# Kernel tuning notes

Measured on AMD Instinct MI355X. Metric: run time of the kernel, lower is better.

## Reference

```python
import jax, jax.numpy as jnp
import numpy as np

KERNEL_MUL = 2.0
KERNEL_NUM = 5


def setup_inputs() -> dict:
    key = jax.random.key(0)
    k1, k2 = jax.random.split(key)
    source = jax.random.normal(k1, (4096, 256), dtype=jnp.float32)
    target = jax.random.normal(k2, (4096, 256), dtype=jnp.float32)
    return {"source": source, "target": target}


def reference(source, target):
    n = source.shape[0]
    m = target.shape[0]
    total = jnp.concatenate([source, target], axis=0)  # [n+m, d]
    N = n + m
    # pairwise squared L2 distances via GEMM identity (same math as expand-based)
    sq = jnp.sum(total * total, axis=1)  # [N]
    d2 = sq[:, None] + sq[None, :] - 2.0 * (total @ total.T)  # [N, N]
    d2 = jnp.maximum(d2, 0.0)
    # bandwidth from detached distances (torch uses L2_distance.data)
    bandwidth = jax.lax.stop_gradient(jnp.sum(d2)) / (N * N - N)
    bandwidth = bandwidth / (KERNEL_MUL ** (KERNEL_NUM // 2))
    kernels = jnp.zeros_like(d2)
    for i in range(KERNEL_NUM):  # fixed small loop over bandwidths
        kernels = kernels + jnp.exp(-d2 / (bandwidth * (KERNEL_MUL ** i)))
    XX = jnp.mean(kernels[:n, :n])
    YY = jnp.mean(kernels[n:, n:])
    XY = jnp.mean(kernels[:n, n:])
    YX = jnp.mean(kernels[n:, :n])
    return XX + YY - XY - YX
```

## Files before the change

### kernel.cpp

```cpp
#include <hip/hip_runtime.h>
#include <hip/hip_bf16.h>
#include <stdint.h>
#include <math.h>

#define D     256
#define NTOT  8192
#define NSRC  4096
#define NT    64
#define NTRI  (NT * (NT + 1) / 2)
#define PREPB 256

using f32x4 = __attribute__((ext_vector_type(4))) float;

#define GLB_AS __attribute__((address_space(1)))
#define LDS_AS __attribute__((address_space(3)))

#if __has_builtin(__builtin_amdgcn_exp2f)
#define EXP2F __builtin_amdgcn_exp2f
#else
#define EXP2F exp2f
#endif

__device__ inline unsigned char f32_to_e4m3(float v) {
  uint32_t u = __float_as_uint(v);
  uint32_t s = (u >> 24) & 0x80u;
  uint32_t m = u & 0x7FFFFFFFu;
  if (m <= 0x3C000000u) return (unsigned char)s;
  if (m <  0x3C800000u) return (unsigned char)(s | 0x08u);
  if (m >= 0x43F00000u) return (unsigned char)(s | 0x7Eu);
  uint32_t r = m + 0x0007FFFFu + ((m >> 20) & 1u);
  uint32_t e = (r >> 23) - 127u + 7u;
  return (unsigned char)(s | (e << 3) | ((r >> 20) & 7u));
}
__device__ inline float e4m3_to_f32(unsigned char q) {
  uint32_t s = ((uint32_t)(q & 0x80u)) << 24;
  uint32_t em = q & 0x7Fu;
  if (em == 0) return __uint_as_float(s);
  uint32_t e = (em >> 3) + 120u;
  return __uint_as_float(s | (e << 23) | ((em & 7u) << 20));
}

__device__ float        g_colsum[256];
__device__ float        g_Ssum;
__device__ unsigned int g_cnt0;
__device__ float        g_cf;

#define OFF_XB   ((size_t)0)
#define OFF_SQ   ((size_t)NTOT * D)
#define OFF_PT   (OFF_SQ + (size_t)NTOT * 4)
#define OFF_END  (OFF_PT + (size_t)NTRI * 4)

__global__ __launch_bounds__(256) void prep_kernel(
    const float* __restrict__ src, const float* __restrict__ tgt,
    unsigned char* __restrict__ xb, float* __restrict__ sq)
{
  __shared__ float scol4[4][256];
  __shared__ float sSl[4];
  __shared__ int slast;
  const int tid = threadIdx.x, wave = tid >> 6, lane = tid & 63;
  const int row0 = blockIdx.x * 32 + wave * 8;
  const float* p0 = (row0 < NSRC) ? (src + (size_t)row0 * D)
                                  : (tgt + (size_t)(row0 - NSRC) * D);
  float c0 = 0.f, c1 = 0.f, c2 = 0.f, c3 = 0.f, swave = 0.f;
  for (int rr = 0; rr < 8; ++rr) {
    const int row = row0 + rr;
    const float4 v = reinterpret_cast<const float4*>(p0 + (size_t)rr * D)[lane];
    uchar4 h;
    h.x = f32_to_e4m3(v.x); h.y = f32_to_e4m3(v.y);
    h.z = f32_to_e4m3(v.z); h.w = f32_to_e4m3(v.w);
    reinterpret_cast<uchar4*>(xb + (size_t)row * D)[lane] = h;
    const float f0 = e4m3_to_f32(h.x), f1 = e4m3_to_f32(h.y),
                f2 = e4m3_to_f32(h.z), f3 = e4m3_to_f32(h.w);
    c0 += f0; c1 += f1; c2 += f2; c3 += f3;
    float s = f0 * f0 + f1 * f1 + f2 * f2 + f3 * f3;
    #pragma unroll
    for (int off = 32; off > 0; off >>= 1) s += __shfl_down(s, off);
    if (lane == 0) { sq[row] = s; swave += s; }
  }
  scol4[wave][lane * 4 + 0] = c0;
  scol4[wave][lane * 4 + 1] = c1;
  scol4[wave][lane * 4 + 2] = c2;
  scol4[wave][lane * 4 + 3] = c3;
  if (lane == 0) sSl[wave] = swave;
  __syncthreads();
  atomicAdd(&g_colsum[tid],
            scol4[0][tid] + scol4[1][tid] + scol4[2][tid] + scol4[3][tid]);
  if (tid == 0) {
    atomicAdd(&g_Ssum, sSl[0] + sSl[1] + sSl[2] + sSl[3]);
    __threadfence();
    slast = (atomicAdd(&g_cnt0, 1u) == (unsigned)(PREPB - 1));
  }
  __syncthreads();
  if (slast) {
    const float cv = atomicExch(&g_colsum[tid], 0.f);
    scol4[0][tid] = cv * cv;
    __syncthreads();
    for (int off = 128; off > 0; off >>= 1) {
      if (tid < off) scol4[0][tid] += scol4[0][tid + off];
      __syncthreads();
    }
    if (tid == 0) {
      const float S = atomicExch(&g_Ssum, 0.f);
      atomicExch(&g_cnt0, 0u);
      const double sumd2 = 2.0 * (double)NTOT * (double)S
                         - 2.0 * (double)scol4[0][0];
      const double bw = sumd2 / ((double)NTOT * (double)NTOT - (double)NTOT) / 4.0;
      g_cf = (float)(-1.4426950408889634 / (bw * 16.0));
    }
  }
}

__global__ __launch_bounds__(256) void pair_kernel(
    const unsigned char* __restrict__ xb, const float* __restrict__ sq,
    float* __restrict__ part)
{
  const int idx = (blockIdx.x & 7) * (NTRI / 8) + (blockIdx.x >> 3);
  const float rr = sqrtf(4160.25f - 2.0f * (float)idx);
  int bi = (int)(64.5f - rr);
  while (NT * (bi + 1) - (bi + 1) * bi / 2 <= idx) ++bi;
  while (NT * bi - bi * (bi - 1) / 2 > idx) --bi;
  const int bj = bi + (idx - (NT * bi - bi * (bi - 1) / 2));

  __shared__ __align__(16) unsigned char lA[128 * 128];
  __shared__ __align__(16) unsigned char lB[128 * 128];
  __shared__ float sqA[128], sqB[128], wsum[4];

  const int tid = threadIdx.x, wave = tid >> 6, lane = tid & 63;
  const int wr = wave >> 1, wc = wave & 1;

  const float c4 = g_cf;
  if (tid < 128) sqA[tid] = sq[bi * 128 + tid];
  else           sqB[tid - 128] = sq[bj * 128 + (tid - 128)];

  const unsigned char* gA0 =
      xb + (size_t)(bi * 128 + wave * 32 + (lane >> 3)) * D + ((lane & 7) ^ (lane >> 3)) * 16;
  const unsigned char* gB0 =
      xb + (size_t)(bj * 128 + wave * 32 + (lane >> 3)) * D + ((lane & 7) ^ (lane >> 3)) * 16;
  char* dA = (char*)lA + wave * 4096;
  char* dB = (char*)lB + wave * 4096;

#define STAGE(t) do {                                                        \
    _Pragma("unroll")                                                        \
    for (int q = 0; q < 4; ++q) {                                            \
      __builtin_amdgcn_global_load_lds(                                      \
          (const GLB_AS uint32_t*)(gA0 + (size_t)q * 8 * D + (t) * 128),     \
          (LDS_AS uint32_t*)(dA + q * 1024), 16, 0, 0);                      \
      __builtin_amdgcn_global_load_lds(                                      \
          (const GLB_AS uint32_t*)(gB0 + (size_t)q * 8 * D + (t) * 128),     \
          (LDS_AS uint32_t*)(dB + q * 1024), 16, 0, 0);                      \
    } } while (0)

  f32x4 acc[4][4];
  #pragma unroll
  for (int mi = 0; mi < 4; ++mi)
    #pragma unroll
    for (int nj = 0; nj < 4; ++nj)
      acc[mi][nj] = (f32x4){0.f, 0.f, 0.f, 0.f};

  const int g = lane >> 4, r7 = lane & 7, rlow = lane & 15;
  const int off8 = (g & 1) * 8, ghalf = g >> 1;

  #pragma unroll
  for (int t = 0; t < 2; ++t) {
    STAGE(t);
    __syncthreads();
    #pragma unroll
    for (int ks = 0; ks < 4; ++ks) {
      const int slot = (2 * ks + ghalf);
      long af[4], bf[4];
      #pragma unroll
      for (int mi = 0; mi < 4; ++mi) {
        const int rowA = wr * 64 + mi * 16 + rlow;
        af[mi] = *(const long*)((const char*)lA + rowA * 128 +
                                (((slot ^ r7)) << 4) + off8);
      }
      #pragma unroll
      for (int nj = 0; nj < 4; ++nj) {
        const int rowB = wc * 64 + nj * 16 + rlow;
        bf[nj] = *(const long*)((const char*)lB + rowB * 128 +
                                (((slot ^ r7)) << 4) + off8);
      }
      #pragma unroll
      for (int mi = 0; mi < 4; ++mi)
        #pragma unroll
        for (int nj = 0; nj < 4; ++nj)
          acc[mi][nj] = __builtin_amdgcn_mfma_f32_16x16x32_fp8_fp8(
              af[mi], bf[nj], acc[mi][nj], 0, 0, 0);
    }
    if (t == 0) __syncthreads();
  }
#undef STAGE

  const int r0c = (lane >> 4) * 4, cc = lane & 15;
  float sjv[4];
  #pragma unroll
  for (int nj = 0; nj < 4; ++nj) sjv[nj] = sqB[wc * 64 + nj * 16 + cc];
  float tsum = 0.f;
  #pragma unroll
  for (int mi = 0; mi < 4; ++mi) {
    #pragma unroll
    for (int r = 0; r < 4; ++r) {
      const float si = sqA[wr * 64 + mi * 16 + r0c + r];
      #pragma unroll
      for (int nj = 0; nj < 4; ++nj) {
        float d2 = fmaf(-2.f, acc[mi][nj][r], si + sjv[nj]);
        d2 = fmaxf(d2, 0.f);
        const float e4 = EXP2F(d2 * c4);
        const float e3 = e4 * e4, e2 = e3 * e3;
        const float e1 = e2 * e2, e0 = e1 * e1;
        tsum += ((e4 + e3) + (e2 + e1)) + e0;
      }
    }
  }
  #pragma unroll
  for (int off = 32; off > 0; off >>= 1) tsum += __shfl_down(tsum, off);
  if (lane == 0) wsum[wave] = tsum;
  __syncthreads();
  if (tid == 0) part[idx] = wsum[0] + wsum[1] + wsum[2] + wsum[3];
}

__global__ __launch_bounds__(256) void out_kernel(
    const float* __restrict__ part, float* __restrict__ out)
{
  __shared__ double red0[256], red1[256], red2[256];
  const int t = threadIdx.x;
  double a0 = 0.0, a1 = 0.0, a2 = 0.0;
  for (int j = t; j < NTRI; j += 256) {
    const float r1 = sqrtf(4160.25f - 2.0f * (float)j);
    int bi = (int)(64.5f - r1);
    while (NT * (bi + 1) - (bi + 1) * bi / 2 <= j) ++bi;
    while (NT * bi - bi * (bi - 1) / 2 > j) --bi;
    const int bj = bi + (j - (NT * bi - bi * (bi - 1) / 2));
    const double w = (bi == bj) ? 1.0 : 2.0;
    const double v = w * (double)part[j];
    if (bi >= 32) a1 += v;
    else if (bj >= 32) a2 += v;
    else a0 += v;
  }
  red0[t] = a0; red1[t] = a1; red2[t] = a2;
  __syncthreads();
  for (int off = 128; off > 0; off >>= 1) {
    if (t < off) {
      red0[t] += red0[t + off];
      red1[t] += red1[t + off];
      red2[t] += red2[t + off];
    }
    __syncthreads();
  }
  if (t == 0)
    out[0] = (float)((red0[0] + red1[0] - red2[0]) /
                     ((double)NSRC * (double)NSRC));
}

extern "C" void kernel_launch(void* const* d_in, const int* in_sizes, int n_in,
                              void* d_out, int out_size, void* d_ws, size_t ws_size,
                              hipStream_t stream) {
  (void)in_sizes; (void)n_in; (void)out_size; (void)ws_size;
  const float* src = (const float*)d_in[0];
  const float* tgt = (const float*)d_in[1];
  char* ws = (char*)d_ws;
  unsigned char* xb = (unsigned char*)(ws + OFF_XB);
  float* sq   = (float*)(ws + OFF_SQ);
  float* part = (float*)(ws + OFF_PT);

  prep_kernel<<<PREPB, 256, 0, stream>>>(src, tgt, xb, sq);
  pair_kernel<<<NTRI, 256, 0, stream>>>(xb, sq, part);
  out_kernel<<<1, 256, 0, stream>>>(part, (float*)d_out);
}
```

Baseline: 52.93 us.

## Spread prep atomics over 8 slots, pack epilogue math, widen final reduction

Prep-kernel column-sum and squared-sum atomics now go to 8 partial slots chosen by block index, which cuts same-address atomic contention; the last block folds the slots together. The pair-kernel epilogue uses 2-wide float vectors for fma, max and the multiplies so the compiler can emit packed FP32 ops. The final out_kernel runs 1024 threads instead of 256 to shorten its serial loop over the partial sums. Exp stays scalar, so the packing only covers part of the epilogue.

```diff
diff --git a/kernel.cpp b/kernel.cpp
--- a/kernel.cpp
+++ b/kernel.cpp
@@ -11,6 +11,7 @@
 #define PREPB 256
 
 using f32x4 = __attribute__((ext_vector_type(4))) float;
+using f32x2 = __attribute__((ext_vector_type(2))) float;
 
 #define GLB_AS __attribute__((address_space(1)))
 #define LDS_AS __attribute__((address_space(3)))
@@ -40,8 +41,8 @@
   return __uint_as_float(s | (e << 23) | ((em & 7u) << 20));
 }
 
-__device__ float        g_colsum[256];
-__device__ float        g_Ssum;
+__device__ float        g_colpart8[8][256];
+__device__ float        g_Ssum8[8];
 __device__ unsigned int g_cnt0;
 __device__ float        g_cf;
 
@@ -83,24 +84,29 @@
   scol4[wave][lane * 4 + 3] = c3;
   if (lane == 0) sSl[wave] = swave;
   __syncthreads();
-  atomicAdd(&g_colsum[tid],
+  atomicAdd(&g_colpart8[blockIdx.x & 7][tid],
             scol4[0][tid] + scol4[1][tid] + scol4[2][tid] + scol4[3][tid]);
   if (tid == 0) {
-    atomicAdd(&g_Ssum, sSl[0] + sSl[1] + sSl[2] + sSl[3]);
+    atomicAdd(&g_Ssum8[blockIdx.x & 7], sSl[0] + sSl[1] + sSl[2] + sSl[3]);
     __threadfence();
     slast = (atomicAdd(&g_cnt0, 1u) == (unsigned)(PREPB - 1));
   }
   __syncthreads();
   if (slast) {
-    const float cv = atomicExch(&g_colsum[tid], 0.f);
-    scol4[0][tid] = cv * cv;
+    float cs = 0.f;
+    #pragma unroll
+    for (int s = 0; s < 8; ++s)
+      cs += atomicExch(&g_colpart8[s][tid], 0.f);
+    scol4[0][tid] = cs * cs;
     __syncthreads();
     for (int off = 128; off > 0; off >>= 1) {
       if (tid < off) scol4[0][tid] += scol4[0][tid + off];
       __syncthreads();
     }
     if (tid == 0) {
-      const float S = atomicExch(&g_Ssum, 0.f);
+      float S = 0.f;
+      #pragma unroll
+      for (int s = 0; s < 8; ++s) S += atomicExch(&g_Ssum8[s], 0.f);
       atomicExch(&g_cnt0, 0u);
       const double sumd2 = 2.0 * (double)NTOT * (double)S
                          - 2.0 * (double)scol4[0][0];
@@ -192,26 +198,34 @@
 #undef STAGE
 
   const int r0c = (lane >> 4) * 4, cc = lane & 15;
+  const f32x2 c42 = (f32x2){c4, c4};
+  const f32x2 n22 = (f32x2){-2.f, -2.f};
+  const f32x2 z2  = (f32x2){0.f, 0.f};
   float sjv[4];
   #pragma unroll
   for (int nj = 0; nj < 4; ++nj) sjv[nj] = sqB[wc * 64 + nj * 16 + cc];
-  float tsum = 0.f;
+  f32x2 tsum2 = z2;
   #pragma unroll
   for (int mi = 0; mi < 4; ++mi) {
     #pragma unroll
-    for (int r = 0; r < 4; ++r) {
-      const float si = sqA[wr * 64 + mi * 16 + r0c + r];
+    for (int p = 0; p < 2; ++p) {
+      const f32x2 si2 = (f32x2){sqA[wr * 64 + mi * 16 + r0c + 2 * p],
+                                sqA[wr * 64 + mi * 16 + r0c + 2 * p + 1]};
       #pragma unroll
       for (int nj = 0; nj < 4; ++nj) {
-        float d2 = fmaf(-2.f, acc[mi][nj][r], si + sjv[nj]);
-        d2 = fmaxf(d2, 0.f);
-        const float e4 = EXP2F(d2 * c4);
-        const float e3 = e4 * e4, e2 = e3 * e3;
-        const float e1 = e2 * e2, e0 = e1 * e1;
-        tsum += ((e4 + e3) + (e2 + e1)) + e0;
+        const f32x2 a2 = (f32x2){acc[mi][nj][2 * p], acc[mi][nj][2 * p + 1]};
+        const f32x2 sj2 = (f32x2){sjv[nj], sjv[nj]};
+        f32x2 d2 = __builtin_elementwise_fma(n22, a2, si2 + sj2);
+        d2 = __builtin_elementwise_max(d2, z2);
+        const f32x2 x2 = d2 * c42;
+        const f32x2 e4 = (f32x2){EXP2F(x2[0]), EXP2F(x2[1])};
+        const f32x2 e3 = e4 * e4, e2v = e3 * e3;
+        const f32x2 e1 = e2v * e2v, e0 = e1 * e1;
+        tsum2 += ((e4 + e3) + (e2v + e1)) + e0;
       }
     }
   }
+  float tsum = tsum2[0] + tsum2[1];
   #pragma unroll
   for (int off = 32; off > 0; off >>= 1) tsum += __shfl_down(tsum, off);
   if (lane == 0) wsum[wave] = tsum;
@@ -219,13 +233,13 @@
   if (tid == 0) part[idx] = wsum[0] + wsum[1] + wsum[2] + wsum[3];
 }
 
-__global__ __launch_bounds__(256) void out_kernel(
+__global__ __launch_bounds__(1024) void out_kernel(
     const float* __restrict__ part, float* __restrict__ out)
 {
-  __shared__ double red0[256], red1[256], red2[256];
+  __shared__ double red0[1024], red1[1024], red2[1024];
   const int t = threadIdx.x;
   double a0 = 0.0, a1 = 0.0, a2 = 0.0;
-  for (int j = t; j < NTRI; j += 256) {
+  for (int j = t; j < NTRI; j += 1024) {
     const float r1 = sqrtf(4160.25f - 2.0f * (float)j);
     int bi = (int)(64.5f - r1);
     while (NT * (bi + 1) - (bi + 1) * bi / 2 <= j) ++bi;
@@ -239,7 +253,7 @@
   }
   red0[t] = a0; red1[t] = a1; red2[t] = a2;
   __syncthreads();
-  for (int off = 128; off > 0; off >>= 1) {
+  for (int off = 512; off > 0; off >>= 1) {
     if (t < off) {
       red0[t] += red0[t + off];
       red1[t] += red1[t + off];
@@ -265,5 +279,5 @@
 
   prep_kernel<<<PREPB, 256, 0, stream>>>(src, tgt, xb, sq);
   pair_kernel<<<NTRI, 256, 0, stream>>>(xb, sq, part);
-  out_kernel<<<1, 256, 0, stream>>>(part, (float*)d_out);
-}
+  out_kernel<<<1, 1024, 0, stream>>>(part, (float*)d_out);
+}
```

Measured after the change: 46.99 us. 1.13x faster.
